# Kernel optimization log

Measured on AMD Instinct MI355X. Metric: run time of the kernel, lower is better.

The kernel has to match this reference:

```python
import jax, jax.numpy as jnp
import numpy as np

H = 128          # hidden_size
D2 = 2 * H       # mod / q_enc channels
D8 = 8 * H       # att channels
B, S, G, Q = 16, 4096, 24, 48
WIN = 12         # +/- window half-width from source


def _masked_softmax(s, m, axis):
    s = jnp.where(m.astype(bool), s, jnp.float32(-1e30))
    return jax.nn.softmax(s, axis=axis)


def _bidaf(c, q, c_mask, q_mask, c_w, q_w, cq_w, bias):
    # c: [B,Lc,D2], q: [B,Lq,D2]; eval mode -> dropout is identity
    s0 = c @ c_w                                  # [B,Lc,1]
    s1 = (q @ q_w).transpose(0, 2, 1)             # [B,1,Lq]
    s2 = jnp.einsum('bcd,bqd->bcq', c * cq_w, q)  # [B,Lc,Lq]
    s = s0 + s1 + s2 + bias
    sm1 = _masked_softmax(s, q_mask[:, None, :], 2)
    sm2 = _masked_softmax(s, c_mask[:, :, None], 1)
    a = jnp.einsum('bcq,bqd->bcd', sm1, q)
    ss = jnp.einsum('bcq,bkq->bck', sm1, sm2)     # s1 @ s2^T
    b = jnp.einsum('bck,bkd->bcd', ss, c)
    return jnp.concatenate([c, a, c * a, c * b], axis=-1)  # [B,Lc,4*D2]


def setup_inputs() -> dict:
    key = jax.random.key(0)
    ks = jax.random.split(key, 12)
    inp = {
        'att': jax.random.normal(ks[0], (B, S, D8), jnp.float32),
        'mod': jax.random.normal(ks[1], (B, S, D2), jnp.float32),
        'q_enc': jax.random.normal(ks[2], (B, Q, D2), jnp.float32),
        'gap_indices': jnp.sort(jax.random.randint(ks[3], (B, G), 0, S), axis=1).astype(jnp.int32),
        'mask': jnp.ones((B, S), jnp.int32),
        'q_mask': jnp.ones((B, Q), jnp.int32),
        'c_w': jax.random.normal(ks[4], (D2, 1), jnp.float32) * 0.05,
        'q_w': jax.random.normal(ks[5], (D2, 1), jnp.float32) * 0.05,
        'cq_w': jax.random.normal(ks[6], (D2,), jnp.float32) * 0.05,
        'att_bias': jnp.zeros((1,), jnp.float32),
        'W_att': jax.random.normal(ks[7], (3 * D8, 1), jnp.float32) * 0.02,
        'b_att': jnp.zeros((1,), jnp.float32),
        'W_mod': jax.random.normal(ks[8], (3 * D2, 1), jnp.float32) * 0.02,
        'b_mod': jnp.zeros((1,), jnp.float32),
        'W_att2': jax.random.normal(ks[9], (D8, 1), jnp.float32) * 0.02,
        'b_att2': jnp.zeros((1,), jnp.float32),
        'W_att_s': jax.random.normal(ks[10], (3 * D8, 1), jnp.float32) * 0.02,
        'b_att_s': jnp.zeros((1,), jnp.float32),
        'W_mod_s': jax.random.normal(ks[11], (3 * D2, 1), jnp.float32) * 0.02,
        'b_mod_s': jnp.zeros((1,), jnp.float32),
        'W_att_s2': jax.random.normal(jax.random.fold_in(key, 99), (D8, 1), jnp.float32) * 0.02,
        'b_att_s2': jnp.zeros((1,), jnp.float32),
    }
    return inp


def reference(att, mod, q_enc, gap_indices, mask, q_mask,
              c_w, q_w, cq_w, att_bias,
              W_att, b_att, W_mod, b_mod, W_att2, b_att2,
              W_att_s, b_att_s, W_mod_s, b_mod_s, W_att_s2, b_att_s2):
    batch, seq_len, _ = mod.shape
    idxb = jnp.arange(batch)[:, None]
    att_gaps = att[idxb, gap_indices]   # [B,G,D8]
    mod_gaps = mod[idxb, gap_indices]   # [B,G,D2]

    att_2 = _bidaf(mod_gaps, q_enc, jnp.ones_like(gap_indices), q_mask,
                   c_w, q_w, cq_w, att_bias)  # [B,G,8h]

    # gap 0: full-sequence pooling (max is unmasked in the source; avg uses mask sum)
    denom0 = jnp.sum(mask.astype(jnp.float32), axis=1)[:, None]
    p0_mod = jnp.concatenate([jnp.max(mod, axis=1), jnp.sum(mod, axis=1) / denom0], axis=-1)[:, None]
    p0_att = jnp.concatenate([jnp.max(att, axis=1), jnp.sum(att, axis=1) / denom0], axis=-1)[:, None]

    pos = jnp.arange(seq_len)[None, :]
    mask_b = mask.astype(bool)

    def step(carry, gid):  # gid: [B]
        wm = (pos >= gid[:, None] - WIN) & (pos <= gid[:, None] + WIN) & mask_b
        wmf = wm.astype(jnp.float32)                 # [B,S]
        den = jnp.sum(wmf, axis=1)[:, None]          # [B,1]
        mw = mod * wmf[:, :, None]
        aw = att * wmf[:, :, None]
        pm = jnp.concatenate([jnp.max(mw, axis=1), jnp.sum(mw, axis=1) / den], axis=-1)
        pa = jnp.concatenate([jnp.max(aw, axis=1), jnp.sum(aw, axis=1) / den], axis=-1)
        return carry, (pm, pa)

    _, (pm, pa) = jax.lax.scan(step, None, gap_indices[:, 1:].T)  # [G-1,B,*]
    pools_mod = jnp.concatenate([p0_mod, pm.transpose(1, 0, 2)], axis=1)  # [B,G,4h]
    pools_att = jnp.concatenate([p0_att, pa.transpose(1, 0, 2)], axis=1)  # [B,G,16h]

    mod_g = jnp.concatenate([mod_gaps, pools_mod], axis=-1)  # [B,G,6h]
    att_g = jnp.concatenate([att_gaps, pools_att], axis=-1)  # [B,G,24h]

    lin = lambda x, W, b: x @ W + b
    logit0 = lin(att_g[:, :1], W_att_s, b_att_s) + lin(mod_g[:, :1], W_mod_s, b_mod_s) + lin(att_2[:, :1], W_att_s2, b_att_s2)
    logits = lin(att_g[:, 1:], W_att, b_att) + lin(mod_g[:, 1:], W_mod, b_mod) + lin(att_2[:, 1:], W_att2, b_att2)
    return jnp.concatenate([logit0, logits], axis=1).squeeze(-1)  # [B,G]
```

## Files before the change

### kernel.cpp

```cpp
#include <hip/hip_runtime.h>
#include <math.h>

#define BATCH 16
#define S_LEN 4096
#define D2c   256
#define D8c   1024
#define GNUM  24
#define QNUM  48
#define WINc  12
#define NCA   64
#define NCM   16
#define NSLOT 64
#define NSB   (BATCH * GNUM)
#define NWB   (BATCH * (GNUM - 1))

__device__ inline float4 f4max(float4 a, float4 b) {
    return make_float4(fmaxf(a.x,b.x), fmaxf(a.y,b.y), fmaxf(a.z,b.z), fmaxf(a.w,b.w));
}
__device__ inline float4 f4add(float4 a, float4 b) {
    return make_float4(a.x+b.x, a.y+b.y, a.z+b.z, a.w+b.w);
}
__device__ inline float4 f4scale(float4 a, float s) {
    return make_float4(a.x*s, a.y*s, a.z*s, a.w*s);
}
__device__ inline float4 f4mul(float4 a, float4 b) {
    return make_float4(a.x*b.x, a.y*b.y, a.z*b.z, a.w*b.w);
}
__device__ inline float dot4(float4 a, float4 b) {
    return a.x*b.x + a.y*b.y + a.z*b.z + a.w*b.w;
}

struct SSh {
    float c[D2c];
    float pa[4][QNUM];
    float pb[4][QNUM];
    float pm[8][32];
    float p0[2][64];
    int   gids[GNUM];
};
struct WSh {
    float wmf[32];
    float red[256];
    float rden;
};
union ShU { SSh s; WSh w; };

__global__ __launch_bounds__(256) void k1_kernel(
    const float* __restrict__ att, const float* __restrict__ mod,
    const float* __restrict__ q_enc,
    const int* __restrict__ gap_idx, const int* __restrict__ mask,
    const float* __restrict__ c_w, const float* __restrict__ cq_w,
    const float* __restrict__ W_att2, const float* __restrict__ W_att_s2,
    const float* __restrict__ W_att, const float* __restrict__ W_mod,
    float* __restrict__ attPmax, float* __restrict__ attPsum,
    float* __restrict__ modPmax, float* __restrict__ modPsum,
    float* __restrict__ s2v_ws, float* __restrict__ vv_ws,
    float* __restrict__ m_ws, float* __restrict__ s0uc_ws,
    float* __restrict__ winpart)
{
    __shared__ ShU sh;
    const int tid = threadIdx.x;
    const int bid = blockIdx.x;

    if (bid < NSB) {
        const int b = bid / GNUM, g = bid % GNUM;
        const float4* mod4 = reinterpret_cast<const float4*>(mod);
        const float4* q4   = reinterpret_cast<const float4*>(q_enc);
        const float4* Wsel = reinterpret_cast<const float4*>((g == 0) ? W_att_s2 : W_att2);

        if (tid < GNUM) sh.s.gids[tid] = gap_idx[b * GNUM + tid];
        __syncthreads();
        const int gid = sh.s.gids[g];
        if (tid < 64)
            reinterpret_cast<float4*>(sh.s.c)[tid] = mod4[((size_t)b * S_LEN + gid) * (D2c/4) + tid];
        __syncthreads();
        const float4* c4 = reinterpret_cast<const float4*>(sh.s.c);

        if (tid < 64) {
            sh.s.p0[0][tid] = dot4(c4[tid], reinterpret_cast<const float4*>(c_w)[tid]);
        } else if (tid < 128) {
            sh.s.p0[1][tid - 64] = dot4(c4[tid - 64], Wsel[tid - 64]);
        }

        {
            const int q = tid & 63, p = tid >> 6;
            if (q < QNUM) {
                const float4* qr = q4 + ((size_t)b * QNUM + q) * (D2c/4) + p * 16;
                const float4* cl = c4 + p * 16;
                const float4* cw = reinterpret_cast<const float4*>(cq_w) + p * 16;
                const float4* wa = Wsel + 2 * (D2c/4) + p * 16;
                float a_s2 = 0.f, a_v = 0.f;
                #pragma unroll
                for (int i = 0; i < 16; ++i) {
                    const float4 cq = f4mul(cl[i], qr[i]);
                    a_s2 += dot4(cq, cw[i]);
                    a_v  += dot4(cq, wa[i]);
                }
                sh.s.pa[p][q] = a_s2;
                sh.s.pb[p][q] = a_v;
            }
        }

        {
            const int k = tid & 31, p8 = tid >> 5;
            if (k < GNUM) {
                const float4* kr = mod4 + ((size_t)b * S_LEN + sh.s.gids[k]) * (D2c/4) + p8 * 8;
                const float4* cl = c4 + p8 * 8;
                const float4* wb = Wsel + 3 * (D2c/4) + p8 * 8;
                float am = 0.f;
                #pragma unroll
                for (int i = 0; i < 8; ++i) {
                    const float4 t = f4mul(cl[i], kr[i]);
                    am += dot4(t, wb[i]);
                }
                sh.s.pm[p8][k] = am;
            }
        }
        __syncthreads();

        if (tid < QNUM) {
            const float s2 = sh.s.pa[0][tid] + sh.s.pa[1][tid] + sh.s.pa[2][tid] + sh.s.pa[3][tid];
            const float v  = sh.s.pb[0][tid] + sh.s.pb[1][tid] + sh.s.pb[2][tid] + sh.s.pb[3][tid];
            s2v_ws[(size_t)bid * QNUM + tid] = s2;
            vv_ws [(size_t)bid * QNUM + tid] = v;
        } else if (tid >= 64 && tid < 64 + GNUM) {
            const int k = tid - 64;
            float m = 0.f;
            #pragma unroll
            for (int p8 = 0; p8 < 8; ++p8) m += sh.s.pm[p8][k];
            m_ws[(size_t)bid * GNUM + k] = m;
        } else if (tid == 62) {
            float a = 0.f;
            for (int i = 0; i < 64; ++i) a += sh.s.p0[0][i];
            s0uc_ws[(size_t)bid * 2 + 0] = a;
        } else if (tid == 63) {
            float a = 0.f;
            for (int i = 0; i < 64; ++i) a += sh.s.p0[1][i];
            s0uc_ws[(size_t)bid * 2 + 1] = a;
        }
    } else if (bid < NSB + NWB) {
        const int wb = bid - NSB;
        const int b = wb / (GNUM - 1), g = wb % (GNUM - 1) + 1;
        const int gid = gap_idx[b * GNUM + g];
        const int lo = (gid - WINc > 0) ? gid - WINc : 0;
        const int hi = (gid + WINc < S_LEN - 1) ? gid + WINc : S_LEN - 1;
        const int n = hi - lo + 1;
        const int gsel = gid - lo;

        if (tid < 32)
            sh.w.wmf[tid] = (tid < n && mask[b * S_LEN + lo + tid] != 0) ? 1.f : 0.f;
        __syncthreads();
        if (tid == 0) {
            float d = 0.f;
            for (int i = 0; i < 25; ++i) d += sh.w.wmf[i];
            sh.w.rden = 1.f / d;
        }
        __syncthreads();
        const float rden = sh.w.rden;

        const float4* Wa4 = reinterpret_cast<const float4*>(W_att);
        const float4* Wm4 = reinterpret_cast<const float4*>(W_mod);

        float acc = 0.f;
        {
            const float4* base = reinterpret_cast<const float4*>(att)
                                 + ((size_t)b * S_LEN + lo) * (D8c/4) + tid;
            float4 mx = make_float4(0.f, 0.f, 0.f, 0.f);
            float4 sm = make_float4(0.f, 0.f, 0.f, 0.f);
            float4 gv = make_float4(0.f, 0.f, 0.f, 0.f);
            #pragma unroll 5
            for (int i = 0; i < 25; ++i) {
                const int off = (i < n) ? i : 0;
                const float4 v = base[(size_t)off * (D8c/4)];
                const float w = sh.w.wmf[i];
                const float4 vm = f4scale(v, w);
                mx = f4max(mx, vm);
                sm = f4add(sm, vm);
                if (i == gsel) gv = v;
            }
            acc += dot4(gv, Wa4[tid]);
            acc += dot4(mx, Wa4[(D8c/4) + tid]) + dot4(sm, Wa4[2*(D8c/4) + tid]) * rden;
        }
        if (tid < D2c/4) {
            const float4* base = reinterpret_cast<const float4*>(mod)
                                 + ((size_t)b * S_LEN + lo) * (D2c/4) + tid;
            float4 mx = make_float4(0.f, 0.f, 0.f, 0.f);
            float4 sm = make_float4(0.f, 0.f, 0.f, 0.f);
            float4 gv = make_float4(0.f, 0.f, 0.f, 0.f);
            #pragma unroll 5
            for (int i = 0; i < 25; ++i) {
                const int off = (i < n) ? i : 0;
                const float4 v = base[(size_t)off * (D2c/4)];
                const float w = sh.w.wmf[i];
                const float4 vm = f4scale(v, w);
                mx = f4max(mx, vm);
                sm = f4add(sm, vm);
                if (i == gsel) gv = v;
            }
            acc += dot4(gv, Wm4[tid]);
            acc += dot4(mx, Wm4[(D2c/4) + tid]) + dot4(sm, Wm4[2*(D2c/4) + tid]) * rden;
        }

        sh.w.red[tid] = acc;
        __syncthreads();
        for (int off = 128; off > 0; off >>= 1) {
            if (tid < off) sh.w.red[tid] += sh.w.red[tid + off];
            __syncthreads();
        }
        if (tid == 0) winpart[b * GNUM + g] = sh.w.red[0];
    } else if (bid < NSB + NWB + BATCH * NCA) {
        const int ab = bid - NSB - NWB;
        const int b = ab >> 6, ch = ab & 63;
        const float4* base = reinterpret_cast<const float4*>(att)
                             + ((size_t)b * S_LEN + ch * 64) * (D8c/4) + tid;
        float4 mx = make_float4(-INFINITY, -INFINITY, -INFINITY, -INFINITY);
        float4 sm = make_float4(0.f, 0.f, 0.f, 0.f);
        #pragma unroll 8
        for (int r = 0; r < 64; ++r) {
            const float4 v = base[(size_t)r * (D8c/4)];
            mx = f4max(mx, v);
            sm = f4add(sm, v);
        }
        reinterpret_cast<float4*>(attPmax)[(size_t)ab * (D8c/4) + tid] = mx;
        reinterpret_cast<float4*>(attPsum)[(size_t)ab * (D8c/4) + tid] = sm;
    } else {
        const int mb = bid - NSB - NWB - BATCH * NCA;
        const int b = mb >> 4, ch = mb & 15;
        const int rg = tid >> 6, c4i = tid & 63;
        const float4* base = reinterpret_cast<const float4*>(mod)
                             + ((size_t)b * S_LEN + ch * 256 + rg * 64) * (D2c/4) + c4i;
        float4 mx = make_float4(-INFINITY, -INFINITY, -INFINITY, -INFINITY);
        float4 sm = make_float4(0.f, 0.f, 0.f, 0.f);
        #pragma unroll 8
        for (int r = 0; r < 64; ++r) {
            const float4 v = base[(size_t)r * (D2c/4)];
            mx = f4max(mx, v);
            sm = f4add(sm, v);
        }
        const int slot = (b * NCM + ch) * 4 + rg;
        reinterpret_cast<float4*>(modPmax)[(size_t)slot * (D2c/4) + c4i] = mx;
        reinterpret_cast<float4*>(modPsum)[(size_t)slot * (D2c/4) + c4i] = sm;
    }
}

__global__ __launch_bounds__(256) void k2_kernel(
    const float* __restrict__ att, const float* __restrict__ mod,
    const float* __restrict__ q_enc,
    const int* __restrict__ gap_idx, const int* __restrict__ mask,
    const int* __restrict__ q_mask,
    const float* __restrict__ q_w, const float* __restrict__ att_bias,
    const float* __restrict__ W_att2, const float* __restrict__ W_att_s2,
    const float* __restrict__ W_att_s, const float* __restrict__ W_mod_s,
    const float* __restrict__ b_att, const float* __restrict__ b_mod,
    const float* __restrict__ b_att2,
    const float* __restrict__ b_att_s, const float* __restrict__ b_mod_s,
    const float* __restrict__ b_att_s2,
    const float* __restrict__ attPmax, const float* __restrict__ attPsum,
    const float* __restrict__ modPmax, const float* __restrict__ modPsum,
    const float* __restrict__ s2v_ws, const float* __restrict__ vv_ws,
    const float* __restrict__ m_ws, const float* __restrict__ s0uc_ws,
    const float* __restrict__ winpart,
    float* __restrict__ out)
{
    const int b = blockIdx.x;
    const int tid = threadIdx.x;

    __shared__ float s_sh[GNUM][QNUM];
    __shared__ float sm1[GNUM][QNUM];
    __shared__ float sm2[GNUM][QNUM];
    __shared__ float ssm[GNUM][GNUM];
    __shared__ float pq[3][4][QNUM];
    __shared__ float s1[QNUM], u0[QNUM], u1[QNUM];
    __shared__ float s0g[GNUM], ucg[GNUM], att2v[GNUM];
    __shared__ float red[256];
    __shared__ float rdensh;

    {
        const int q = tid & 63, p = tid >> 6;
        if (q < QNUM) {
            const float4* qr = reinterpret_cast<const float4*>(q_enc)
                               + ((size_t)b * QNUM + q) * (D2c/4) + p * 16;
            const float4* w1 = reinterpret_cast<const float4*>(q_w) + p * 16;
            const float4* w2 = reinterpret_cast<const float4*>(W_att_s2) + (D2c/4) + p * 16;
            const float4* w3 = reinterpret_cast<const float4*>(W_att2)   + (D2c/4) + p * 16;
            float a1 = 0.f, a2 = 0.f, a3 = 0.f;
            #pragma unroll
            for (int i = 0; i < 16; ++i) {
                const float4 v = qr[i];
                a1 += dot4(v, w1[i]);
                a2 += dot4(v, w2[i]);
                a3 += dot4(v, w3[i]);
            }
            pq[0][p][q] = a1; pq[1][p][q] = a2; pq[2][p][q] = a3;
        }
    }
    if (tid < GNUM) {
        s0g[tid] = s0uc_ws[((size_t)b * GNUM + tid) * 2 + 0];
        ucg[tid] = s0uc_ws[((size_t)b * GNUM + tid) * 2 + 1];
    }
    __syncthreads();
    if (tid < QNUM) {
        s1[tid] = pq[0][0][tid] + pq[0][1][tid] + pq[0][2][tid] + pq[0][3][tid];
        u0[tid] = pq[1][0][tid] + pq[1][1][tid] + pq[1][2][tid] + pq[1][3][tid];
        u1[tid] = pq[2][0][tid] + pq[2][1][tid] + pq[2][2][tid] + pq[2][3][tid];
    }
    __syncthreads();

    const float bias = att_bias[0];
    for (int i = tid; i < GNUM * QNUM; i += 256) {
        const int g = i / QNUM, q = i % QNUM;
        s_sh[g][q] = s0g[g] + s1[q] + s2v_ws[((size_t)b * GNUM + g) * QNUM + q] + bias;
    }
    __syncthreads();

    if (tid < QNUM) {
        const int q = tid;
        float mxv = -1e30f;
        for (int g = 0; g < GNUM; ++g) mxv = fmaxf(mxv, s_sh[g][q]);
        float sum = 0.f;
        for (int g = 0; g < GNUM; ++g) {
            const float e = __expf(s_sh[g][q] - mxv);
            sm2[g][q] = e;
            sum += e;
        }
        const float inv = 1.f / sum;
        for (int g = 0; g < GNUM; ++g) sm2[g][q] *= inv;
    } else if (tid >= 64 && tid < 64 + GNUM) {
        const int g = tid - 64;
        float mxv = -1e30f;
        for (int q = 0; q < QNUM; ++q)
            if (q_mask[b * QNUM + q]) mxv = fmaxf(mxv, s_sh[g][q]);
        float sum = 0.f;
        for (int q = 0; q < QNUM; ++q) {
            const float e = q_mask[b * QNUM + q] ? __expf(s_sh[g][q] - mxv) : 0.f;
            sm1[g][q] = e;
            sum += e;
        }
        const float inv = 1.f / sum;
        for (int q = 0; q < QNUM; ++q) sm1[g][q] *= inv;
    }
    __syncthreads();

    for (int i = tid; i < GNUM * GNUM; i += 256) {
        const int g = i / GNUM, k = i % GNUM;
        float t = 0.f;
        for (int q = 0; q < QNUM; ++q) t += sm1[g][q] * sm2[k][q];
        ssm[g][k] = t * m_ws[((size_t)b * GNUM + g) * GNUM + k];
    }
    __syncthreads();

    if (tid < GNUM) {
        const int g = tid;
        const float* uu = (g == 0) ? u0 : u1;
        float acc = ucg[g];
        for (int q = 0; q < QNUM; ++q)
            acc += sm1[g][q] * (uu[q] + vv_ws[((size_t)b * GNUM + g) * QNUM + q]);
        for (int k = 0; k < GNUM; ++k) acc += ssm[g][k];
        att2v[g] = acc;
    }

    float cnt = 0.f;
    for (int s = tid; s < S_LEN; s += 256) cnt += (mask[b * S_LEN + s] != 0) ? 1.f : 0.f;
    red[tid] = cnt;
    __syncthreads();
    for (int off = 128; off > 0; off >>= 1) {
        if (tid < off) red[tid] += red[tid + off];
        __syncthreads();
    }
    if (tid == 0) rdensh = 1.f / red[0];
    __syncthreads();
    const float rden0 = rdensh;

    const int gid0 = gap_idx[b * GNUM];
    const float4* Wa4 = reinterpret_cast<const float4*>(W_att_s);
    const float4* Wm4 = reinterpret_cast<const float4*>(W_mod_s);

    float acc = 0.f;
    {
        float4 mx = make_float4(-INFINITY, -INFINITY, -INFINITY, -INFINITY);
        float4 sm = make_float4(0.f, 0.f, 0.f, 0.f);
        #pragma unroll 8
        for (int ch = 0; ch < NSLOT; ++ch) {
            const size_t idx = ((size_t)b * NSLOT + ch) * (D8c/4) + tid;
            mx = f4max(mx, reinterpret_cast<const float4*>(attPmax)[idx]);
            sm = f4add(sm, reinterpret_cast<const float4*>(attPsum)[idx]);
        }
        acc += dot4(mx, Wa4[(D8c/4) + tid]) + dot4(sm, Wa4[2*(D8c/4) + tid]) * rden0;
        const float4 ar = reinterpret_cast<const float4*>(att)[((size_t)b * S_LEN + gid0) * (D8c/4) + tid];
        acc += dot4(ar, Wa4[tid]);
    }
    if (tid < D2c/4) {
        float4 mx = make_float4(-INFINITY, -INFINITY, -INFINITY, -INFINITY);
        float4 sm = make_float4(0.f, 0.f, 0.f, 0.f);
        #pragma unroll 8
        for (int ch = 0; ch < NSLOT; ++ch) {
            const size_t idx = ((size_t)b * NSLOT + ch) * (D2c/4) + tid;
            mx = f4max(mx, reinterpret_cast<const float4*>(modPmax)[idx]);
            sm = f4add(sm, reinterpret_cast<const float4*>(modPsum)[idx]);
        }
        acc += dot4(mx, Wm4[(D2c/4) + tid]) + dot4(sm, Wm4[2*(D2c/4) + tid]) * rden0;
        const float4 mr = reinterpret_cast<const float4*>(mod)[((size_t)b * S_LEN + gid0) * (D2c/4) + tid];
        acc += dot4(mr, Wm4[tid]);
    }

    __syncthreads();
    red[tid] = acc;
    __syncthreads();
    for (int off = 128; off > 0; off >>= 1) {
        if (tid < off) red[tid] += red[tid + off];
        __syncthreads();
    }
    if (tid == 0) {
        out[b * GNUM] = red[0] + att2v[0] + b_att_s[0] + b_mod_s[0] + b_att_s2[0];
    } else if (tid < GNUM) {
        out[b * GNUM + tid] = winpart[b * GNUM + tid] + att2v[tid]
                              + b_att[0] + b_mod[0] + b_att2[0];
    }
}

extern "C" void kernel_launch(void* const* d_in, const int* in_sizes, int n_in,
                              void* d_out, int out_size, void* d_ws, size_t ws_size,
                              hipStream_t stream)
{
    const float* att      = (const float*)d_in[0];
    const float* mod      = (const float*)d_in[1];
    const float* q_enc    = (const float*)d_in[2];
    const int*   gap_idx  = (const int*)  d_in[3];
    const int*   mask     = (const int*)  d_in[4];
    const int*   q_mask   = (const int*)  d_in[5];
    const float* c_w      = (const float*)d_in[6];
    const float* q_w      = (const float*)d_in[7];
    const float* cq_w     = (const float*)d_in[8];
    const float* att_bias = (const float*)d_in[9];
    const float* W_att    = (const float*)d_in[10];
    const float* b_att    = (const float*)d_in[11];
    const float* W_mod    = (const float*)d_in[12];
    const float* b_mod    = (const float*)d_in[13];
    const float* W_att2   = (const float*)d_in[14];
    const float* b_att2   = (const float*)d_in[15];
    const float* W_att_s  = (const float*)d_in[16];
    const float* b_att_s  = (const float*)d_in[17];
    const float* W_mod_s  = (const float*)d_in[18];
    const float* b_mod_s  = (const float*)d_in[19];
    const float* W_att_s2 = (const float*)d_in[20];
    const float* b_att_s2 = (const float*)d_in[21];

    float* out = (float*)d_out;

    float* ws = (float*)d_ws;
    float* attPmax = ws;
    float* attPsum = attPmax + (size_t)BATCH * NSLOT * D8c;
    float* modPmax = attPsum + (size_t)BATCH * NSLOT * D8c;
    float* modPsum = modPmax + (size_t)BATCH * NSLOT * D2c;
    float* s2v_ws  = modPsum + (size_t)BATCH * NSLOT * D2c;
    float* vv_ws   = s2v_ws  + (size_t)NSB * QNUM;
    float* m_ws    = vv_ws   + (size_t)NSB * QNUM;
    float* s0uc_ws = m_ws    + (size_t)NSB * GNUM;
    float* winpart = s0uc_ws + (size_t)NSB * 2;

    const int grid1 = NSB + NWB + BATCH*NCA + BATCH*NCM;

    k1_kernel<<<grid1, 256, 0, stream>>>(
        att, mod, q_enc, gap_idx, mask,
        c_w, cq_w, W_att2, W_att_s2, W_att, W_mod,
        attPmax, attPsum, modPmax, modPsum,
        s2v_ws, vv_ws, m_ws, s0uc_ws, winpart);

    k2_kernel<<<BATCH, 256, 0, stream>>>(
        att, mod, q_enc, gap_idx, mask, q_mask,
        q_w, att_bias, W_att2, W_att_s2,
        W_att_s, W_mod_s, b_att, b_mod, b_att2,
        b_att_s, b_mod_s, b_att_s2,
        attPmax, attPsum, modPmax, modPsum,
        s2v_ws, vv_ws, m_ws, s0uc_ws, winpart, out);
}
```

Baseline: 106.8 us.

## Reduce full-sequence pool via atomics and fold the average into per-chunk dot products

The chunk-reduction blocks no longer write per-chunk partial max and sum vectors to workspace. The max is now combined with atomicMax on order-preserving unsigned encodings of the floats. The sum is dotted with the average-pool weights inside each block, block-reduced and added into a per-batch scalar with atomicAdd. This removes the 64-slot final reduction loop from the 16-block second kernel, which was a serial tail over several MB of partials. In exchange it adds a memset launch and atomic contention, and the float atomicAdd makes the summation order nondeterministic.

```diff
diff --git a/kernel.cpp b/kernel.cpp
--- a/kernel.cpp
+++ b/kernel.cpp
@@ -10,7 +10,6 @@
 #define WINc  12
 #define NCA   64
 #define NCM   16
-#define NSLOT 64
 #define NSB   (BATCH * GNUM)
 #define NWB   (BATCH * (GNUM - 1))
 
@@ -28,6 +27,13 @@
 }
 __device__ inline float dot4(float4 a, float4 b) {
     return a.x*b.x + a.y*b.y + a.z*b.z + a.w*b.w;
+}
+__device__ inline unsigned fmap(float x) {
+    unsigned u = __float_as_uint(x);
+    return (u >> 31) ? ~u : (u | 0x80000000u);
+}
+__device__ inline float funmap(unsigned u) {
+    return (u >> 31) ? __uint_as_float(u & 0x7FFFFFFFu) : __uint_as_float(~u);
 }
 
 struct SSh {
@@ -52,8 +58,9 @@
     const float* __restrict__ c_w, const float* __restrict__ cq_w,
     const float* __restrict__ W_att2, const float* __restrict__ W_att_s2,
     const float* __restrict__ W_att, const float* __restrict__ W_mod,
-    float* __restrict__ attPmax, float* __restrict__ attPsum,
-    float* __restrict__ modPmax, float* __restrict__ modPsum,
+    const float* __restrict__ W_att_s, const float* __restrict__ W_mod_s,
+    unsigned* __restrict__ attMaxU, unsigned* __restrict__ modMaxU,
+    float* __restrict__ sumdots,
     float* __restrict__ s2v_ws, float* __restrict__ vv_ws,
     float* __restrict__ m_ws, float* __restrict__ s0uc_ws,
     float* __restrict__ winpart)
@@ -221,8 +228,19 @@
             mx = f4max(mx, v);
             sm = f4add(sm, v);
         }
-        reinterpret_cast<float4*>(attPmax)[(size_t)ab * (D8c/4) + tid] = mx;
-        reinterpret_cast<float4*>(attPsum)[(size_t)ab * (D8c/4) + tid] = sm;
+        unsigned* amax = attMaxU + (size_t)b * D8c + tid * 4;
+        atomicMax(&amax[0], fmap(mx.x));
+        atomicMax(&amax[1], fmap(mx.y));
+        atomicMax(&amax[2], fmap(mx.z));
+        atomicMax(&amax[3], fmap(mx.w));
+        const float4 wsum = reinterpret_cast<const float4*>(W_att_s)[2*(D8c/4) + tid];
+        sh.w.red[tid] = dot4(sm, wsum);
+        __syncthreads();
+        for (int off = 128; off > 0; off >>= 1) {
+            if (tid < off) sh.w.red[tid] += sh.w.red[tid + off];
+            __syncthreads();
+        }
+        if (tid == 0) atomicAdd(&sumdots[b], sh.w.red[0]);
     } else {
         const int mb = bid - NSB - NWB - BATCH * NCA;
         const int b = mb >> 4, ch = mb & 15;
@@ -237,9 +255,19 @@
             mx = f4max(mx, v);
             sm = f4add(sm, v);
         }
-        const int slot = (b * NCM + ch) * 4 + rg;
-        reinterpret_cast<float4*>(modPmax)[(size_t)slot * (D2c/4) + c4i] = mx;
-        reinterpret_cast<float4*>(modPsum)[(size_t)slot * (D2c/4) + c4i] = sm;
+        unsigned* mmax = modMaxU + (size_t)b * D2c + c4i * 4;
+        atomicMax(&mmax[0], fmap(mx.x));
+        atomicMax(&mmax[1], fmap(mx.y));
+        atomicMax(&mmax[2], fmap(mx.z));
+        atomicMax(&mmax[3], fmap(mx.w));
+        const float4 wsum = reinterpret_cast<const float4*>(W_mod_s)[2*(D2c/4) + c4i];
+        sh.w.red[tid] = dot4(sm, wsum);
+        __syncthreads();
+        for (int off = 128; off > 0; off >>= 1) {
+            if (tid < off) sh.w.red[tid] += sh.w.red[tid + off];
+            __syncthreads();
+        }
+        if (tid == 0) atomicAdd(&sumdots[BATCH + b], sh.w.red[0]);
     }
 }
 
@@ -255,8 +283,8 @@
     const float* __restrict__ b_att2,
     const float* __restrict__ b_att_s, const float* __restrict__ b_mod_s,
     const float* __restrict__ b_att_s2,
-    const float* __restrict__ attPmax, const float* __restrict__ attPsum,
-    const float* __restrict__ modPmax, const float* __restrict__ modPsum,
+    const unsigned* __restrict__ attMaxU, const unsigned* __restrict__ modMaxU,
+    const float* __restrict__ sumdots,
     const float* __restrict__ s2v_ws, const float* __restrict__ vv_ws,
     const float* __restrict__ m_ws, const float* __restrict__ s0uc_ws,
     const float* __restrict__ winpart,
@@ -377,28 +405,16 @@
 
     float acc = 0.f;
     {
-        float4 mx = make_float4(-INFINITY, -INFINITY, -INFINITY, -INFINITY);
-        float4 sm = make_float4(0.f, 0.f, 0.f, 0.f);
-        #pragma unroll 8
-        for (int ch = 0; ch < NSLOT; ++ch) {
-            const size_t idx = ((size_t)b * NSLOT + ch) * (D8c/4) + tid;
-            mx = f4max(mx, reinterpret_cast<const float4*>(attPmax)[idx]);
-            sm = f4add(sm, reinterpret_cast<const float4*>(attPsum)[idx]);
-        }
-        acc += dot4(mx, Wa4[(D8c/4) + tid]) + dot4(sm, Wa4[2*(D8c/4) + tid]) * rden0;
+        const uint4 mu = reinterpret_cast<const uint4*>(attMaxU + (size_t)b * D8c)[tid];
+        const float4 mx = make_float4(funmap(mu.x), funmap(mu.y), funmap(mu.z), funmap(mu.w));
+        acc += dot4(mx, Wa4[(D8c/4) + tid]);
         const float4 ar = reinterpret_cast<const float4*>(att)[((size_t)b * S_LEN + gid0) * (D8c/4) + tid];
         acc += dot4(ar, Wa4[tid]);
     }
     if (tid < D2c/4) {
-        float4 mx = make_float4(-INFINITY, -INFINITY, -INFINITY, -INFINITY);
-        float4 sm = make_float4(0.f, 0.f, 0.f, 0.f);
-        #pragma unroll 8
-        for (int ch = 0; ch < NSLOT; ++ch) {
-            const size_t idx = ((size_t)b * NSLOT + ch) * (D2c/4) + tid;
-            mx = f4max(mx, reinterpret_cast<const float4*>(modPmax)[idx]);
-            sm = f4add(sm, reinterpret_cast<const float4*>(modPsum)[idx]);
-        }
-        acc += dot4(mx, Wm4[(D2c/4) + tid]) + dot4(sm, Wm4[2*(D2c/4) + tid]) * rden0;
+        const uint4 mu = reinterpret_cast<const uint4*>(modMaxU + (size_t)b * D2c)[tid];
+        const float4 mx = make_float4(funmap(mu.x), funmap(mu.y), funmap(mu.z), funmap(mu.w));
+        acc += dot4(mx, Wm4[(D2c/4) + tid]);
         const float4 mr = reinterpret_cast<const float4*>(mod)[((size_t)b * S_LEN + gid0) * (D2c/4) + tid];
         acc += dot4(mr, Wm4[tid]);
     }
@@ -411,7 +427,8 @@
         __syncthreads();
     }
     if (tid == 0) {
-        out[b * GNUM] = red[0] + att2v[0] + b_att_s[0] + b_mod_s[0] + b_att_s2[0];
+        const float avgpart = (sumdots[b] + sumdots[BATCH + b]) * rden0;
+        out[b * GNUM] = red[0] + avgpart + att2v[0] + b_att_s[0] + b_mod_s[0] + b_att_s2[0];
     } else if (tid < GNUM) {
         out[b * GNUM + tid] = winpart[b * GNUM + tid] + att2v[tid]
                               + b_att[0] + b_mod[0] + b_att2[0];
@@ -447,23 +464,24 @@
 
     float* out = (float*)d_out;
 
-    float* ws = (float*)d_ws;
-    float* attPmax = ws;
-    float* attPsum = attPmax + (size_t)BATCH * NSLOT * D8c;
-    float* modPmax = attPsum + (size_t)BATCH * NSLOT * D8c;
-    float* modPsum = modPmax + (size_t)BATCH * NSLOT * D2c;
-    float* s2v_ws  = modPsum + (size_t)BATCH * NSLOT * D2c;
-    float* vv_ws   = s2v_ws  + (size_t)NSB * QNUM;
-    float* m_ws    = vv_ws   + (size_t)NSB * QNUM;
-    float* s0uc_ws = m_ws    + (size_t)NSB * GNUM;
-    float* winpart = s0uc_ws + (size_t)NSB * 2;
+    unsigned* attMaxU = (unsigned*)d_ws;
+    unsigned* modMaxU = attMaxU + (size_t)BATCH * D8c;
+    float*    sumdots = (float*)(modMaxU + (size_t)BATCH * D2c);
+    float*    s2v_ws  = sumdots + 32;
+    float*    vv_ws   = s2v_ws + (size_t)NSB * QNUM;
+    float*    m_ws    = vv_ws  + (size_t)NSB * QNUM;
+    float*    s0uc_ws = m_ws   + (size_t)NSB * GNUM;
+    float*    winpart = s0uc_ws + (size_t)NSB * 2;
+
+    const size_t atomicBytes = ((size_t)BATCH * D8c + (size_t)BATCH * D2c + 32) * 4;
+    hipMemsetAsync(d_ws, 0, atomicBytes, stream);
 
     const int grid1 = NSB + NWB + BATCH*NCA + BATCH*NCM;
 
     k1_kernel<<<grid1, 256, 0, stream>>>(
         att, mod, q_enc, gap_idx, mask,
-        c_w, cq_w, W_att2, W_att_s2, W_att, W_mod,
-        attPmax, attPsum, modPmax, modPsum,
+        c_w, cq_w, W_att2, W_att_s2, W_att, W_mod, W_att_s, W_mod_s,
+        attMaxU, modMaxU, sumdots,
         s2v_ws, vv_ws, m_ws, s0uc_ws, winpart);
 
     k2_kernel<<<BATCH, 256, 0, stream>>>(
@@ -471,6 +489,6 @@
         q_w, att_bias, W_att2, W_att_s2,
         W_att_s, W_mod_s, b_att, b_mod, b_att2,
         b_att_s, b_mod_s, b_att_s2,
-        attPmax, attPsum, modPmax, modPsum,
+        attMaxU, modMaxU, sumdots,
         s2v_ws, vv_ws, m_ws, s0uc_ws, winpart, out);
 }
```

Result: faster. 100.9 us (-5.5%).
